# Kernel optimization log

Measured on AMD Instinct MI355X. Metric: run time of the kernel, lower is better.

## Reference

```python
import jax, jax.numpy as jnp
import numpy as np

D_MODEL = 64

def setup_inputs() -> dict:
    key = jax.random.key(0)
    k1, k2, k3, k4 = jax.random.split(key, 4)
    B, T, E = 4, 4096, 128
    x = jax.random.normal(k1, (B, T, E), dtype=jnp.float32)
    # nn.Linear weights, stored transposed as (in, out) for x @ W
    s = 1.0 / np.sqrt(E)
    Wq = jax.random.uniform(k2, (E, D_MODEL), jnp.float32, -s, s)
    Wk = jax.random.uniform(k3, (E, D_MODEL), jnp.float32, -s, s)
    Wv = jax.random.uniform(k4, (E, D_MODEL), jnp.float32, -s, s)
    return {"x": x, "Wq": Wq, "Wk": Wk, "Wv": Wv}

def reference(x, Wq, Wk, Wv):
    B, T, E = x.shape
    q = jnp.einsum('bte,ed->btd', x, Wq)
    k = jnp.einsum('bte,ed->btd', x, Wk)
    v = jnp.einsum('bte,ed->btd', x, Wv)
    scores = jnp.einsum('bqd,bkd->bqk', q, k) / np.sqrt(D_MODEL)  # [B,T,T]
    causal = jnp.tril(jnp.ones((T, T), dtype=bool))
    scores = jnp.where(causal, scores, jnp.float32(-1e9))
    attn = jax.nn.softmax(scores, axis=-1)
    # dropout p=0.0 -> identity (eval-mode faithful)
    return jnp.einsum('bqk,bkd->bqd', attn, v)
```

## Files before the change

kernel.cpp:

```cpp
#include <hip/hip_runtime.h>
#include <hip/hip_bf16.h>


typedef __attribute__((ext_vector_type(4))) float  f32x4;
typedef __attribute__((ext_vector_type(4))) unsigned int u32x4;
typedef __attribute__((ext_vector_type(8))) __bf16 bf16x8;
typedef __attribute__((ext_vector_type(8))) unsigned short u16x8;
typedef __attribute__((ext_vector_type(4))) unsigned short u16x4;

#define T_SEQ 4096
#define DH    64
#define EDIM  128
#define KVB   64
#define KSTR  72
#define VSTR  136
#define QSCALE 0.18033688f
#define NTRI  528

__device__ __forceinline__ unsigned short f2bf(float f) {
    unsigned int x = __builtin_bit_cast(unsigned int, f);
    unsigned int r = x + 0x7fffu + ((x >> 16) & 1u);
    return (unsigned short)(r >> 16);
}

__device__ __forceinline__ unsigned int cvt_pk_bf16(float lo, float hi) {
    unsigned int d;
    asm("v_cvt_pk_bf16_f32 %0, %1, %2" : "=v"(d) : "v"(lo), "v"(hi));
    return d;
}

__device__ __forceinline__ f32x4 mfma_bf16(u16x8 a, u16x8 b, f32x4 c) {
    return __builtin_amdgcn_mfma_f32_16x16x32_bf16(
        __builtin_bit_cast(bf16x8, a), __builtin_bit_cast(bf16x8, b), c, 0, 0, 0);
}

__global__ __launch_bounds__(256) void prep_w_kernel(
    const float* __restrict__ wq, const float* __restrict__ wk,
    const float* __restrict__ wv, unsigned short* __restrict__ wt)
{
    int o = blockIdx.x * 256 + threadIdx.x;
    int m   = o >> 13;
    int rem = o & 8191;
    int d = rem >> 7, e = rem & 127;
    const float* W = (m == 0) ? wq : (m == 1) ? wk : wv;
    wt[o] = f2bf(W[e * DH + d]);
}

__global__ __launch_bounds__(64) void proj_kernel(
    const float* __restrict__ x, const unsigned short* __restrict__ wt,
    unsigned short* __restrict__ qw, unsigned short* __restrict__ kw,
    unsigned short* __restrict__ vt)
{
    const int l   = threadIdx.x;
    const int l15 = l & 15;
    const int lg  = l >> 4;
    const int row0 = blockIdx.x * 16;
    const int b    = row0 >> 12;
    const int t0   = row0 & 4095;

    u16x8 af[4];
    #pragma unroll
    for (int kt = 0; kt < 4; ++kt) {
        const float* xp = x + (row0 + l15) * EDIM + kt * 32 + lg * 8;
        f32x4 a = *(const f32x4*)xp;
        f32x4 bb = *(const f32x4*)(xp + 4);
        af[kt] = u16x8{ f2bf(a[0]), f2bf(a[1]), f2bf(a[2]), f2bf(a[3]),
                        f2bf(bb[0]), f2bf(bb[1]), f2bf(bb[2]), f2bf(bb[3]) };
    }

    unsigned short* outs[2] = { qw, kw };
    #pragma unroll
    for (int m = 0; m < 2; ++m) {
        #pragma unroll
        for (int nt = 0; nt < 4; ++nt) {
            f32x4 acc = {};
            #pragma unroll
            for (int kt = 0; kt < 4; ++kt) {
                u16x8 bfrag = *(const u16x8*)(wt + (m * 64 + nt * 16 + l15) * EDIM
                                                 + kt * 32 + lg * 8);
                acc = mfma_bf16(af[kt], bfrag, acc);
            }
            const float sc = (m == 0) ? QSCALE : 1.0f;
            #pragma unroll
            for (int r = 0; r < 4; ++r)
                outs[m][(row0 + lg * 4 + r) * DH + nt * 16 + l15] = f2bf(acc[r] * sc);
        }
    }

    #pragma unroll
    for (int nt = 0; nt < 4; ++nt) {
        f32x4 acc = {};
        #pragma unroll
        for (int kt = 0; kt < 4; ++kt) {
            u16x8 bfrag = *(const u16x8*)(wt + (2 * 64 + nt * 16 + l15) * EDIM
                                             + kt * 32 + lg * 8);
            acc = mfma_bf16(af[kt], bfrag, acc);
        }
        u16x4 pv = { f2bf(acc[0]), f2bf(acc[1]), f2bf(acc[2]), f2bf(acc[3]) };
        *(u16x4*)(vt + ((size_t)(b * DH + nt * 16 + l15)) * T_SEQ + t0 + lg * 4) = pv;
    }
}

__global__ __launch_bounds__(256, 4) void attn_partial_kernel(
    const unsigned short* __restrict__ qg, const unsigned short* __restrict__ kg,
    const unsigned short* __restrict__ vt,
    unsigned short* __restrict__ po, float* __restrict__ pm, float* __restrict__ pl)
{
    const int bid = blockIdx.x;
    const int b   = bid / NTRI;
    const int i   = bid - b * NTRI;
    int q = (int)((__builtin_sqrtf((float)(8 * i + 1)) - 1.0f) * 0.5f);
    while (q * (q + 1) / 2 > i) --q;
    while ((q + 1) * (q + 2) / 2 <= i) ++q;
    const int q128 = q;
    const int ch   = i - q * (q + 1) / 2;

    __shared__ unsigned short K_lds[128 * KSTR];
    __shared__ unsigned short V_lds[64 * VSTR];

    const int tid = threadIdx.x;
    const int w   = tid >> 6;
    const int l   = tid & 63;
    const int l15 = l & 15;
    const int lg  = l >> 4;

    const int base   = b * T_SEQ;
    const int qrow0w = q128 * 128 + w * 32;
    const int kvb    = ch * 128;

    const unsigned short* kgB = kg + (size_t)base * DH;
    const unsigned short* vtB = vt + (size_t)b * DH * T_SEQ;

    {
        u16x8 kr[4], vr[4];
        #pragma unroll
        for (int j = 0; j < 4; ++j) {
            int gi = tid + j * 256;
            kr[j] = *(const u16x8*)(kgB + (size_t)(kvb + (gi >> 3)) * DH + (gi & 7) * 8);
            vr[j] = *(const u16x8*)(vtB + (size_t)(gi >> 4) * T_SEQ + kvb + (gi & 15) * 8);
        }
        #pragma unroll
        for (int j = 0; j < 4; ++j) {
            int gi = tid + j * 256;
            *(u16x8*)&K_lds[(gi >> 3) * KSTR + (gi & 7) * 8] = kr[j];
            *(u16x8*)&V_lds[(gi >> 4) * VSTR + (gi & 15) * 8] = vr[j];
        }
    }

    u16x8 qf[2][2];
    #pragma unroll
    for (int rt = 0; rt < 2; ++rt) {
        const unsigned short* qrow = qg + (base + qrow0w + rt * 16 + l15) * DH;
        qf[rt][0] = *(const u16x8*)(qrow + 0 + lg * 8);
        qf[rt][1] = *(const u16x8*)(qrow + 32 + lg * 8);
    }

    f32x4 o_acc[2][4];
    float m_run[2], l_run[2];
    #pragma unroll
    for (int rt = 0; rt < 2; ++rt) {
        #pragma unroll
        for (int dt = 0; dt < 4; ++dt) o_acc[rt][dt] = f32x4{};
        m_run[rt] = -1e30f; l_run[rt] = 0.0f;
    }

    const int src0 = l15 + 32 * (lg & 1);
    const int src1 = src0 + 16;
    const bool hi  = (lg >> 1) != 0;

    __syncthreads();

    #pragma unroll
    for (int tt = 0; tt < 2; ++tt) {
        const int kv0 = kvb + tt * 64;
        if (kv0 > qrow0w + 31) continue;
        const unsigned short* Kt = K_lds + (tt * 64) * KSTR;
        const unsigned short* Vt = V_lds + tt * 64;

        u16x8 kf[4][2];
        #pragma unroll
        for (int nt = 0; nt < 4; ++nt)
            #pragma unroll
            for (int kt = 0; kt < 2; ++kt)
                kf[nt][kt] = *(const u16x8*)&Kt[(nt * 16 + l15) * KSTR
                                                + kt * 32 + lg * 8];

        f32x4 s[2][4];
        __builtin_amdgcn_s_setprio(1);
        #pragma unroll
        for (int rt = 0; rt < 2; ++rt)
            #pragma unroll
            for (int nt = 0; nt < 4; ++nt) {
                f32x4 a = {};
                a = mfma_bf16(kf[nt][0], qf[rt][0], a);
                a = mfma_bf16(kf[nt][1], qf[rt][1], a);
                s[rt][nt] = a;
            }
        __builtin_amdgcn_s_setprio(0);

        if (kv0 + KVB - 1 > qrow0w) {
            #pragma unroll
            for (int rt = 0; rt < 2; ++rt)
                #pragma unroll
                for (int nt = 0; nt < 4; ++nt)
                    #pragma unroll
                    for (int rr = 0; rr < 4; ++rr) {
                        int kj = kv0 + nt * 16 + lg * 4 + rr;
                        int qi = qrow0w + rt * 16 + l15;
                        if (kj > qi) s[rt][nt][rr] = -1e30f;
                    }
        }

        float sc2[2];
        bool grow = false;
        unsigned int pk[2][4][2];
        #pragma unroll
        for (int rt = 0; rt < 2; ++rt) {
            float mx = s[rt][0][0];
            #pragma unroll
            for (int nt = 0; nt < 4; ++nt)
                #pragma unroll
                for (int rr = 0; rr < 4; ++rr)
                    mx = fmaxf(mx, s[rt][nt][rr]);
            mx = fmaxf(mx, __shfl_xor(mx, 16));
            mx = fmaxf(mx, __shfl_xor(mx, 32));

            float mold = m_run[rt];
            float mnew = fmaxf(mold, mx);
            grow |= (mx > mold);
            float sc = exp2f(mold - mnew);
            sc2[rt] = sc;
            m_run[rt] = mnew;

            float rs = 0.0f;
            #pragma unroll
            for (int nt = 0; nt < 4; ++nt)
                #pragma unroll
                for (int rr = 0; rr < 4; ++rr) {
                    float p = exp2f(s[rt][nt][rr] - mnew);
                    s[rt][nt][rr] = p;
                    rs += p;
                }
            rs += __shfl_xor(rs, 16);
            rs += __shfl_xor(rs, 32);
            l_run[rt] = l_run[rt] * sc + rs;

            #pragma unroll
            for (int nt = 0; nt < 4; ++nt) {
                pk[rt][nt][0] = cvt_pk_bf16(s[rt][nt][0], s[rt][nt][1]);
                pk[rt][nt][1] = cvt_pk_bf16(s[rt][nt][2], s[rt][nt][3]);
            }
        }
        if (__any(grow)) {
            #pragma unroll
            for (int rt = 0; rt < 2; ++rt)
                #pragma unroll
                for (int dt = 0; dt < 4; ++dt)
                    o_acc[rt][dt] *= sc2[rt];
        }

        __builtin_amdgcn_s_setprio(1);
        #pragma unroll
        for (int kt = 0; kt < 2; ++kt) {
            u16x8 vf[4];
            #pragma unroll
            for (int dt = 0; dt < 4; ++dt)
                vf[dt] = *(const u16x8*)&Vt[(dt * 16 + l15) * VSTR
                                            + kt * 32 + lg * 8];
            #pragma unroll
            for (int rt = 0; rt < 2; ++rt) {
                unsigned int pb[4];
                #pragma unroll
                for (int t = 0; t < 4; ++t) {
                    int src = (t < 2) ? src0 : src1;
                    unsigned int pa  = __shfl(pk[rt][2 * kt][t & 1], src);
                    unsigned int pbv = __shfl(pk[rt][2 * kt + 1][t & 1], src);
                    pb[t] = hi ? pbv : pa;
                }
                u32x4 pbq = { pb[0], pb[1], pb[2], pb[3] };
                u16x8 pbf = __builtin_bit_cast(u16x8, pbq);
                #pragma unroll
                for (int dt = 0; dt < 4; ++dt)
                    o_acc[rt][dt] = mfma_bf16(vf[dt], pbf, o_acc[rt][dt]);
            }
        }
        __builtin_amdgcn_s_setprio(0);
    }

    const int pidx = bid;
    unsigned short* pob = po + (size_t)pidx * 8192;
    #pragma unroll
    for (int rt = 0; rt < 2; ++rt) {
        int row = w * 32 + rt * 16 + l15;
        #pragma unroll
        for (int dt = 0; dt < 4; ++dt) {
            unsigned int w0 = cvt_pk_bf16(o_acc[rt][dt][0], o_acc[rt][dt][1]);
            unsigned int w1 = cvt_pk_bf16(o_acc[rt][dt][2], o_acc[rt][dt][3]);
            *(unsigned int*)&pob[row * 64 + dt * 16 + lg * 4]     = w0;
            *(unsigned int*)&pob[row * 64 + dt * 16 + lg * 4 + 2] = w1;
        }
        if (lg == 0) {
            pm[pidx * 128 + row] = m_run[rt];
            pl[pidx * 128 + row] = l_run[rt];
        }
    }
}

__global__ __launch_bounds__(256) void attn_combine_kernel(
    const unsigned short* __restrict__ po, const float* __restrict__ pm,
    const float* __restrict__ pl, float* __restrict__ out)
{
    const int blk   = blockIdx.x;
    const int slice = blk & 3;
    const int tb    = blk >> 2;
    const int q128  = tb & 31;
    const int b     = tb >> 5;
    const int nch   = q128 + 1;
    const int bslot = b * NTRI + q128 * (q128 + 1) / 2;
    const int row   = slice * 32 + (threadIdx.x >> 3);
    const int d0    = (threadIdx.x & 7) * 8;

    float mstar = -1e30f;
    for (int i = 0; i < nch; ++i)
        mstar = fmaxf(mstar, pm[(bslot + i) * 128 + row]);

    float lsum = 0.0f;
    float a[8] = {};
    for (int i = 0; i < nch; ++i) {
        float wi = exp2f(pm[(bslot + i) * 128 + row] - mstar);
        lsum += wi * pl[(bslot + i) * 128 + row];
        u16x8 v = *(const u16x8*)&po[(size_t)(bslot + i) * 8192 + row * 64 + d0];
        #pragma unroll
        for (int j = 0; j < 8; ++j) {
            unsigned int u = (unsigned int)v[j] << 16;
            a[j] += wi * __builtin_bit_cast(float, u);
        }
    }
    const float inv = 1.0f / lsum;
    float* op = out + (size_t)(b * T_SEQ + q128 * 128 + row) * DH + d0;
    f32x4 o0 = { a[0] * inv, a[1] * inv, a[2] * inv, a[3] * inv };
    f32x4 o1 = { a[4] * inv, a[5] * inv, a[6] * inv, a[7] * inv };
    *(f32x4*)op = o0;
    *(f32x4*)(op + 4) = o1;
}

__global__ __launch_bounds__(64, 4) void attn_direct_kernel(
    const unsigned short* __restrict__ qg, const unsigned short* __restrict__ kg,
    const unsigned short* __restrict__ vt, float* __restrict__ out)
{
    const int bid = blockIdx.x;
    const int q32 = bid & 127;
    const int b   = bid >> 7;
    const int l = threadIdx.x, l15 = l & 15, lg = l >> 4;
    const int qrow0 = q32 * 32;
    const int base  = b * T_SEQ;
    const unsigned short* kp = kg + (size_t)base * DH;
    const unsigned short* vp = vt + (size_t)b * DH * T_SEQ;

    u16x8 qf[2][2];
    #pragma unroll
    for (int rt = 0; rt < 2; ++rt) {
        const unsigned short* qrow = qg + (base + qrow0 + rt * 16 + l15) * DH;
        qf[rt][0] = *(const u16x8*)(qrow + 0 + lg * 8);
        qf[rt][1] = *(const u16x8*)(qrow + 32 + lg * 8);
    }

    f32x4 o_acc[2][4];
    float m_run[2], l_run[2];
    #pragma unroll
    for (int rt = 0; rt < 2; ++rt) {
        #pragma unroll
        for (int dt = 0; dt < 4; ++dt) o_acc[rt][dt] = f32x4{};
        m_run[rt] = -1e30f; l_run[rt] = 0.0f;
    }

    const int src0 = l15 + 32 * (lg & 1);
    const int src1 = src0 + 16;
    const bool hi  = (lg >> 1) != 0;

    for (int kv0 = 0; kv0 <= qrow0 + 31; kv0 += KVB) {
        u16x8 kf[4][2];
        #pragma unroll
        for (int nt = 0; nt < 4; ++nt)
            #pragma unroll
            for (int kt = 0; kt < 2; ++kt)
                kf[nt][kt] = *(const u16x8*)(kp + (kv0 + nt * 16 + l15) * DH
                                                + kt * 32 + lg * 8);
        f32x4 s[2][4];
        #pragma unroll
        for (int rt = 0; rt < 2; ++rt)
            #pragma unroll
            for (int nt = 0; nt < 4; ++nt) {
                f32x4 a = {};
                a = mfma_bf16(kf[nt][0], qf[rt][0], a);
                a = mfma_bf16(kf[nt][1], qf[rt][1], a);
                s[rt][nt] = a;
            }
        if (kv0 + KVB - 1 > qrow0) {
            #pragma unroll
            for (int rt = 0; rt < 2; ++rt)
                #pragma unroll
                for (int nt = 0; nt < 4; ++nt)
                    #pragma unroll
                    for (int rr = 0; rr < 4; ++rr) {
                        int kj = kv0 + nt * 16 + lg * 4 + rr;
                        int qi = qrow0 + rt * 16 + l15;
                        if (kj > qi) s[rt][nt][rr] = -1e30f;
                    }
        }
        float sc2[2];
        bool grow = false;
        unsigned int pk[2][4][2];
        #pragma unroll
        for (int rt = 0; rt < 2; ++rt) {
            float mx = s[rt][0][0];
            #pragma unroll
            for (int nt = 0; nt < 4; ++nt)
                #pragma unroll
                for (int rr = 0; rr < 4; ++rr)
                    mx = fmaxf(mx, s[rt][nt][rr]);
            mx = fmaxf(mx, __shfl_xor(mx, 16));
            mx = fmaxf(mx, __shfl_xor(mx, 32));
            float mold = m_run[rt];
            float mnew = fmaxf(mold, mx);
            grow |= (mx > mold);
            float sc = exp2f(mold - mnew);
            sc2[rt] = sc;
            m_run[rt] = mnew;
            float rs = 0.0f;
            #pragma unroll
            for (int nt = 0; nt < 4; ++nt)
                #pragma unroll
                for (int rr = 0; rr < 4; ++rr) {
                    float p = exp2f(s[rt][nt][rr] - mnew);
                    s[rt][nt][rr] = p;
                    rs += p;
                }
            rs += __shfl_xor(rs, 16);
            rs += __shfl_xor(rs, 32);
            l_run[rt] = l_run[rt] * sc + rs;
            #pragma unroll
            for (int nt = 0; nt < 4; ++nt) {
                pk[rt][nt][0] = cvt_pk_bf16(s[rt][nt][0], s[rt][nt][1]);
                pk[rt][nt][1] = cvt_pk_bf16(s[rt][nt][2], s[rt][nt][3]);
            }
        }
        if (__any(grow)) {
            #pragma unroll
            for (int rt = 0; rt < 2; ++rt)
                #pragma unroll
                for (int dt = 0; dt < 4; ++dt)
                    o_acc[rt][dt] *= sc2[rt];
        }
        #pragma unroll
        for (int kt = 0; kt < 2; ++kt) {
            u16x8 vf[4];
            #pragma unroll
            for (int dt = 0; dt < 4; ++dt)
                vf[dt] = *(const u16x8*)(vp + (size_t)(dt * 16 + l15) * T_SEQ
                                            + kv0 + kt * 32 + lg * 8);
            #pragma unroll
            for (int rt = 0; rt < 2; ++rt) {
                unsigned int pb[4];
                #pragma unroll
                for (int t = 0; t < 4; ++t) {
                    int src = (t < 2) ? src0 : src1;
                    unsigned int pa  = __shfl(pk[rt][2 * kt][t & 1], src);
                    unsigned int pbv = __shfl(pk[rt][2 * kt + 1][t & 1], src);
                    pb[t] = hi ? pbv : pa;
                }
                u32x4 pbq = { pb[0], pb[1], pb[2], pb[3] };
                u16x8 pbf = __builtin_bit_cast(u16x8, pbq);
                #pragma unroll
                for (int dt = 0; dt < 4; ++dt)
                    o_acc[rt][dt] = mfma_bf16(vf[dt], pbf, o_acc[rt][dt]);
            }
        }
    }

    #pragma unroll
    for (int rt = 0; rt < 2; ++rt) {
        float inv = 1.0f / l_run[rt];
        int row = base + qrow0 + rt * 16 + l15;
        #pragma unroll
        for (int dt = 0; dt < 4; ++dt) {
            f32x4 ov = o_acc[rt][dt] * inv;
            *(f32x4*)&out[(size_t)row * DH + dt * 16 + lg * 4] = ov;
        }
    }
}

extern "C" void kernel_launch(void* const* d_in, const int* in_sizes, int n_in,
                              void* d_out, int out_size, void* d_ws, size_t ws_size,
                              hipStream_t stream)
{
    const float* x  = (const float*)d_in[0];
    const float* wq = (const float*)d_in[1];
    const float* wk = (const float*)d_in[2];
    const float* wv = (const float*)d_in[3];
    float* out = (float*)d_out;

    unsigned short* wt = (unsigned short*)d_ws;
    unsigned short* qw = (unsigned short*)((char*)d_ws + 65536);
    unsigned short* kw = qw + (size_t)16384 * DH;
    unsigned short* vt = kw + (size_t)16384 * DH;

    const size_t slots  = 4u * NTRI;
    const size_t po_off = 65536u + 3u * 16384u * DH * 2u;
    const size_t po_sz  = slots * 8192 * 2;
    const size_t pm_off = po_off + po_sz;
    const size_t pl_off = pm_off + slots * 128 * 4;
    const size_t need   = pl_off + slots * 128 * 4;

    prep_w_kernel<<<96, 256, 0, stream>>>(wq, wk, wv, wt);
    proj_kernel<<<1024, 64, 0, stream>>>(x, wt, qw, kw, vt);

    if (ws_size >= need) {
        unsigned short* po = (unsigned short*)((char*)d_ws + po_off);
        float* pm = (float*)((char*)d_ws + pm_off);
        float* pl = (float*)((char*)d_ws + pl_off);
        attn_partial_kernel<<<4 * NTRI, 256, 0, stream>>>(qw, kw, vt, po, pm, pl);
        attn_combine_kernel<<<4 * 32 * 4, 256, 0, stream>>>(po, pm, pl, out);
    } else {
        attn_direct_kernel<<<4 * 128, 64, 0, stream>>>(qw, kw, vt, out);
    }
}
```

Baseline: 63.91 us.

## Swizzle K/V shared-memory layout, raise occupancy, unroll combine loads

Replaces the padded K and V shared-memory tiles with XOR-swizzled unpadded layouts. This reduces LDS footprint and is meant to avoid bank conflicts on the 16-byte fragment reads. The shrink allows the launch-bounds occupancy hint to go from 4 to 5 blocks. The combine kernel now fully unrolls over up to 32 chunks and preloads all partial maxima, exposing more memory-level parallelism at the cost of extra registers and predicated code.

```diff
diff --git a/kernel.cpp b/kernel.cpp
--- a/kernel.cpp
+++ b/kernel.cpp
@@ -12,8 +12,6 @@
 #define DH    64
 #define EDIM  128
 #define KVB   64
-#define KSTR  72
-#define VSTR  136
 #define QSCALE 0.18033688f
 #define NTRI  528
 
@@ -32,6 +30,13 @@
 __device__ __forceinline__ f32x4 mfma_bf16(u16x8 a, u16x8 b, f32x4 c) {
     return __builtin_amdgcn_mfma_f32_16x16x32_bf16(
         __builtin_bit_cast(bf16x8, a), __builtin_bit_cast(bf16x8, b), c, 0, 0, 0);
+}
+
+__device__ __forceinline__ int kswz(int row, int bcol) {
+    return row * 128 + (bcol ^ ((row & 7) << 4));
+}
+__device__ __forceinline__ int vswz(int row, int bcol) {
+    return row * 256 + (bcol ^ ((row & 15) << 4));
 }
 
 __global__ __launch_bounds__(256) void prep_w_kernel(
@@ -101,7 +106,7 @@
     }
 }
 
-__global__ __launch_bounds__(256, 4) void attn_partial_kernel(
+__global__ __launch_bounds__(256, 5) void attn_partial_kernel(
     const unsigned short* __restrict__ qg, const unsigned short* __restrict__ kg,
     const unsigned short* __restrict__ vt,
     unsigned short* __restrict__ po, float* __restrict__ pm, float* __restrict__ pl)
@@ -115,8 +120,8 @@
     const int q128 = q;
     const int ch   = i - q * (q + 1) / 2;
 
-    __shared__ unsigned short K_lds[128 * KSTR];
-    __shared__ unsigned short V_lds[64 * VSTR];
+    __shared__ char K_ldsb[128 * 128];
+    __shared__ char V_ldsb[64 * 256];
 
     const int tid = threadIdx.x;
     const int w   = tid >> 6;
@@ -142,8 +147,8 @@
         #pragma unroll
         for (int j = 0; j < 4; ++j) {
             int gi = tid + j * 256;
-            *(u16x8*)&K_lds[(gi >> 3) * KSTR + (gi & 7) * 8] = kr[j];
-            *(u16x8*)&V_lds[(gi >> 4) * VSTR + (gi & 15) * 8] = vr[j];
+            *(u16x8*)&K_ldsb[kswz(gi >> 3, (gi & 7) * 16)]  = kr[j];
+            *(u16x8*)&V_ldsb[vswz(gi >> 4, (gi & 15) * 16)] = vr[j];
         }
     }
 
@@ -174,16 +179,15 @@
     for (int tt = 0; tt < 2; ++tt) {
         const int kv0 = kvb + tt * 64;
         if (kv0 > qrow0w + 31) continue;
-        const unsigned short* Kt = K_lds + (tt * 64) * KSTR;
-        const unsigned short* Vt = V_lds + tt * 64;
 
         u16x8 kf[4][2];
         #pragma unroll
         for (int nt = 0; nt < 4; ++nt)
             #pragma unroll
-            for (int kt = 0; kt < 2; ++kt)
-                kf[nt][kt] = *(const u16x8*)&Kt[(nt * 16 + l15) * KSTR
-                                                + kt * 32 + lg * 8];
+            for (int kt = 0; kt < 2; ++kt) {
+                int krow = tt * 64 + nt * 16 + l15;
+                kf[nt][kt] = *(const u16x8*)&K_ldsb[kswz(krow, kt * 64 + lg * 16)];
+            }
 
         f32x4 s[2][4];
         __builtin_amdgcn_s_setprio(1);
@@ -264,9 +268,10 @@
         for (int kt = 0; kt < 2; ++kt) {
             u16x8 vf[4];
             #pragma unroll
-            for (int dt = 0; dt < 4; ++dt)
-                vf[dt] = *(const u16x8*)&Vt[(dt * 16 + l15) * VSTR
-                                            + kt * 32 + lg * 8];
+            for (int dt = 0; dt < 4; ++dt) {
+                int vrow = dt * 16 + l15;
+                vf[dt] = *(const u16x8*)&V_ldsb[vswz(vrow, tt * 128 + kt * 64 + lg * 16)];
+            }
             #pragma unroll
             for (int rt = 0; rt < 2; ++rt) {
                 unsigned int pb[4];
@@ -320,20 +325,30 @@
     const int row   = slice * 32 + (threadIdx.x >> 3);
     const int d0    = (threadIdx.x & 7) * 8;
 
-    float mstar = -1e30f;
-    for (int i = 0; i < nch; ++i)
-        mstar = fmaxf(mstar, pm[(bslot + i) * 128 + row]);
+    float m_i[32];
+    #pragma unroll
+    for (int i = 0; i < 32; ++i) {
+        int ii = (i < nch) ? i : 0;
+        m_i[i] = pm[(bslot + ii) * 128 + row];
+    }
+    float mstar = m_i[0];
+    #pragma unroll
+    for (int i = 1; i < 32; ++i)
+        if (i < nch) mstar = fmaxf(mstar, m_i[i]);
 
     float lsum = 0.0f;
     float a[8] = {};
-    for (int i = 0; i < nch; ++i) {
-        float wi = exp2f(pm[(bslot + i) * 128 + row] - mstar);
-        lsum += wi * pl[(bslot + i) * 128 + row];
-        u16x8 v = *(const u16x8*)&po[(size_t)(bslot + i) * 8192 + row * 64 + d0];
-        #pragma unroll
-        for (int j = 0; j < 8; ++j) {
-            unsigned int u = (unsigned int)v[j] << 16;
-            a[j] += wi * __builtin_bit_cast(float, u);
+    #pragma unroll
+    for (int i = 0; i < 32; ++i) {
+        if (i < nch) {
+            float wi = exp2f(m_i[i] - mstar);
+            lsum += wi * pl[(bslot + i) * 128 + row];
+            u16x8 v = *(const u16x8*)&po[(size_t)(bslot + i) * 8192 + row * 64 + d0];
+            #pragma unroll
+            for (int j = 0; j < 8; ++j) {
+                unsigned int u = (unsigned int)v[j] << 16;
+                a[j] += wi * __builtin_bit_cast(float, u);
+            }
         }
     }
     const float inv = 1.0f / lsum;
```

Result: slower. 82.00 us (+28.3%).
